# Kernel tuning notes

Measured on AMD Instinct MI355X. Metric: run time of the kernel, lower is better.

Reference implementation:

```python
import jax, jax.numpy as jnp
import numpy as np


def _tent(t):
    # linear interpolation kernel max(1-|t|, 0)
    return jnp.maximum(1.0 - jnp.abs(t), 0.0)


def _slice_coeffs(grid, guide):
    """Trilinear slice of bilateral grid at guide-dependent depth.
    grid: [B, C, D, GH, GW], guide: [B, H, W] in [0,1] -> coeffs [B, C, H, W]."""
    B, C, D, GH, GW = grid.shape
    _, H, W = guide.shape
    # continuous grid coords (HDRNet convention)
    gx = (jnp.arange(W, dtype=guide.dtype) + 0.5) * (GW / W)      # [W]
    gy = (jnp.arange(H, dtype=guide.dtype) + 0.5) * (GH / H)      # [H]
    gz = guide * D                                                # [B,H,W]
    fx = jnp.floor(gx - 0.5)
    fy = jnp.floor(gy - 0.5)
    fz = jnp.floor(gz - 0.5)

    def gather(g, z, y, x):
        # g: [C,D,GH,GW]; z,y,x: [B? broadcasted per-batch] -> [C,H,W]
        return g[:, z, y, x]

    coeffs = jnp.zeros((B, C, H, W), dtype=grid.dtype)
    ones_bhw = jnp.ones_like(gz)
    for dz in (0, 1):
        zz = fz + dz                                   # [B,H,W]
        wz = _tent(gz - 0.5 - zz)                      # [B,H,W]
        zc = jnp.clip(zz, 0, D - 1).astype(jnp.int32)
        for dy in (0, 1):
            yy = fy + dy                               # [H]
            wy = _tent(gy - 0.5 - yy)                  # [H]
            yc = jnp.clip(yy, 0, GH - 1).astype(jnp.int32)
            for dx in (0, 1):
                xx = fx + dx                           # [W]
                wx = _tent(gx - 0.5 - xx)              # [W]
                xc = jnp.clip(xx, 0, GW - 1).astype(jnp.int32)
                # broadcast indices to [B,H,W]
                Y = jnp.broadcast_to(yc[None, :, None], zc.shape)
                X = jnp.broadcast_to(xc[None, None, :], zc.shape)
                corner = jax.vmap(gather)(grid, zc, Y, X)   # [B,C,H,W]
                w = wz * wy[None, :, None] * wx[None, None, :]  # [B,H,W]
                coeffs = coeffs + corner * w[:, None, :, :]
    return coeffs


def reference(grid, guide, image):
    B, C, D, GH, GW = grid.shape
    n_out = image.shape[1]               # 3
    n_aff = C // n_out                   # n_in + 1 = 4
    coeffs = _slice_coeffs(grid, guide)  # [B, C, H, W]
    coeffs = coeffs.reshape(B, n_out, n_aff, *image.shape[2:])  # [B,3,4,H,W]
    # per-pixel affine: out_c = sum_i A[c,i] * img_i + A[c, n_in]
    out = jnp.einsum('bcihw,bihw->bchw', coeffs[:, :, : n_aff - 1], image)
    out = out + coeffs[:, :, n_aff - 1]
    return out


def setup_inputs() -> dict:
    key = jax.random.key(0)
    k1, k2, k3 = jax.random.split(key, 3)
    grid = jax.random.normal(k1, (4, 12, 8, 16, 16), dtype=jnp.float32)
    guide = jax.random.uniform(k2, (4, 1024, 1024), dtype=jnp.float32)
    image = jax.random.uniform(k3, (4, 3, 1024, 1024), dtype=jnp.float32)
    return {"grid": grid, "guide": guide, "image": image}
```

## Files before the change

### kernel.cpp

```cpp
#include <hip/hip_runtime.h>


static constexpr int C_ = 12, D_ = 8, GH_ = 16, GW_ = 16;
static constexpr int H_ = 1024, W_ = 1024;
static constexpr int HW_ = H_ * W_;
static constexpr int XS = D_ * C_ + 4;

__global__ __launch_bounds__(256) void bsa_row_kernel(
    const float* __restrict__ grid,
    const float* __restrict__ guide,
    const float* __restrict__ image,
    float* __restrict__ out)
{
    __shared__ float s[GW_ * XS];

    const int bid = blockIdx.x;
    const int y = bid & (H_ - 1);
    const int b = bid >> 10;
    const int t = threadIdx.x;

    const float gyc = (y + 0.5f) * (1.0f / 64.0f) - 0.5f;
    const float fy = floorf(gyc);
    const float ty = gyc - fy;
    const int iy = (int)fy;
    const int y0 = min(max(iy, 0), GH_ - 1);
    const int y1 = min(max(iy + 1, 0), GH_ - 1);

    const int sx = t & 15, sc = t >> 4;
    float sv0[8], sv1[8];
    const float* gb = grid + b * (C_ * D_ * GH_ * GW_);
    if (t < 192) {
        const int base = sc * (D_ * GH_ * GW_) + sx;
#pragma unroll
        for (int z = 0; z < 8; ++z) {
            sv0[z] = gb[base + z * (GH_ * GW_) + y0 * GW_];
            sv1[z] = gb[base + z * (GH_ * GW_) + y1 * GW_];
        }
    }

    const float* gdp = guide + (size_t)bid * W_;
    const float* imp = image + (size_t)b * 3 * HW_ + (size_t)y * W_;
    float gz4[4], r4[4], g4[4], b4[4];
#pragma unroll
    for (int j = 0; j < 4; ++j) {
        const int p = j * 256 + t;
        gz4[j] = gdp[p];
        r4[j]  = imp[p];
        g4[j]  = imp[HW_ + p];
        b4[j]  = imp[2 * HW_ + p];
    }

    if (t < 192) {
#pragma unroll
        for (int z = 0; z < 8; ++z)
            s[sx * XS + z * C_ + sc] = sv0[z] + ty * (sv1[z] - sv0[z]);
    }
    __syncthreads();

    float* const ob = out + (size_t)b * 3 * HW_ + (size_t)y * W_;
#pragma unroll
    for (int j = 0; j < 4; ++j) {
        const int p = j * 256 + t;

        const float gxc = (p + 0.5f) * (1.0f / 64.0f) - 0.5f;
        const float fx = floorf(gxc);
        const float tx = gxc - fx;
        const int ix = (int)fx;
        const int x0 = min(max(ix, 0), GW_ - 1);
        const int x1 = min(max(ix + 1, 0), GW_ - 1);

        const float gz = gz4[j] * (float)D_ - 0.5f;
        const float fz = floorf(gz);
        const float tz = gz - fz;
        const int iz = (int)fz;
        const int z0 = min(max(iz, 0), D_ - 1);
        const int z1 = min(max(iz + 1, 0), D_ - 1);

        const float w00 = (1.f - tx) * (1.f - tz);
        const float w01 = (1.f - tx) * tz;
        const float w10 = tx * (1.f - tz);
        const float w11 = tx * tz;

        const float* p00 = s + x0 * XS + z0 * C_;
        const float* p01 = s + x0 * XS + z1 * C_;
        const float* p10 = s + x1 * XS + z0 * C_;
        const float* p11 = s + x1 * XS + z1 * C_;

        const float rv = r4[j], gv = g4[j], bv = b4[j];

#pragma unroll
        for (int k = 0; k < 3; ++k) {
            float4 a0 = *(const float4*)(p00 + 4 * k);
            float4 a1 = *(const float4*)(p01 + 4 * k);
            float4 a2 = *(const float4*)(p10 + 4 * k);
            float4 a3 = *(const float4*)(p11 + 4 * k);
            float cx = w00 * a0.x + w01 * a1.x + w10 * a2.x + w11 * a3.x;
            float cy = w00 * a0.y + w01 * a1.y + w10 * a2.y + w11 * a3.y;
            float cz = w00 * a0.z + w01 * a1.z + w10 * a2.z + w11 * a3.z;
            float cw = w00 * a0.w + w01 * a1.w + w10 * a2.w + w11 * a3.w;
            ob[k * HW_ + p] = cx * rv + cy * gv + cz * bv + cw;
        }
    }
}

extern "C" void kernel_launch(void* const* d_in, const int* in_sizes, int n_in,
                              void* d_out, int out_size, void* d_ws, size_t ws_size,
                              hipStream_t stream) {
    const float* grid  = (const float*)d_in[0];
    const float* guide = (const float*)d_in[1];
    const float* image = (const float*)d_in[2];
    float* out = (float*)d_out;

    bsa_row_kernel<<<4 * H_, 256, 0, stream>>>(grid, guide, image, out);
}
```

Baseline: 24.44 us.

## Pack z-adjacent grid values as half2 in LDS to halve slice loads

Stores each shared-memory grid entry as a half2 holding the value at depth z and z+1, so a pixel's trilinear slice needs two 16-byte LDS reads per group of four coefficients instead of four. The z interpolation is then done from the packed pair, and the edge cases are handled by clamping z0 and zeroing tz. This cuts LDS traffic and address arithmetic in a kernel that is likely bound by memory bandwidth. In exchange it adds fp16 conversions and rounds the grid coefficients to half precision, which lowers accuracy.

```diff
diff --git a/kernel.cpp b/kernel.cpp
--- a/kernel.cpp
+++ b/kernel.cpp
@@ -1,4 +1,5 @@
 #include <hip/hip_runtime.h>
+#include <hip/hip_fp16.h>
 
 
 static constexpr int C_ = 12, D_ = 8, GH_ = 16, GW_ = 16;
@@ -6,13 +7,13 @@
 static constexpr int HW_ = H_ * W_;
 static constexpr int XS = D_ * C_ + 4;
 
-__global__ __launch_bounds__(256) void bsa_row_kernel(
+__global__ __launch_bounds__(256) void bsa_h2_kernel(
     const float* __restrict__ grid,
     const float* __restrict__ guide,
     const float* __restrict__ image,
     float* __restrict__ out)
 {
-    __shared__ float s[GW_ * XS];
+    __shared__ __half2 s[GW_ * XS];
 
     const int bid = blockIdx.x;
     const int y = bid & (H_ - 1);
@@ -51,9 +52,17 @@
     }
 
     if (t < 192) {
+        float a[8];
 #pragma unroll
         for (int z = 0; z < 8; ++z)
-            s[sx * XS + z * C_ + sc] = sv0[z] + ty * (sv1[z] - sv0[z]);
+            a[z] = sv0[z] + ty * (sv1[z] - sv0[z]);
+        const int sl = sx * XS + sc;
+#pragma unroll
+        for (int z = 0; z < 8; ++z) {
+            const int zn = (z < 7) ? z + 1 : 7;
+            s[sl + z * C_] = __halves2half2(__float2half_rn(a[z]),
+                                            __float2half_rn(a[zn]));
+        }
     }
     __syncthreads();
 
@@ -71,35 +80,37 @@
 
         const float gz = gz4[j] * (float)D_ - 0.5f;
         const float fz = floorf(gz);
-        const float tz = gz - fz;
         const int iz = (int)fz;
-        const int z0 = min(max(iz, 0), D_ - 1);
-        const int z1 = min(max(iz + 1, 0), D_ - 1);
+        const float tz = (iz < 0) ? 0.0f : (gz - fz);
+        const int z0 = max(iz, 0);
 
-        const float w00 = (1.f - tx) * (1.f - tz);
-        const float w01 = (1.f - tx) * tz;
-        const float w10 = tx * (1.f - tz);
-        const float w11 = tx * tz;
-
-        const float* p00 = s + x0 * XS + z0 * C_;
-        const float* p01 = s + x0 * XS + z1 * C_;
-        const float* p10 = s + x1 * XS + z0 * C_;
-        const float* p11 = s + x1 * XS + z1 * C_;
+        const __half2* q0 = s + x0 * XS + z0 * C_;
+        const __half2* q1 = s + x1 * XS + z0 * C_;
 
         const float rv = r4[j], gv = g4[j], bv = b4[j];
+        float res[3];
 
 #pragma unroll
         for (int k = 0; k < 3; ++k) {
-            float4 a0 = *(const float4*)(p00 + 4 * k);
-            float4 a1 = *(const float4*)(p01 + 4 * k);
-            float4 a2 = *(const float4*)(p10 + 4 * k);
-            float4 a3 = *(const float4*)(p11 + 4 * k);
-            float cx = w00 * a0.x + w01 * a1.x + w10 * a2.x + w11 * a3.x;
-            float cy = w00 * a0.y + w01 * a1.y + w10 * a2.y + w11 * a3.y;
-            float cz = w00 * a0.z + w01 * a1.z + w10 * a2.z + w11 * a3.z;
-            float cw = w00 * a0.w + w01 * a1.w + w10 * a2.w + w11 * a3.w;
-            ob[k * HW_ + p] = cx * rv + cy * gv + cz * bv + cw;
+            float4 u0 = *(const float4*)(q0 + 4 * k);
+            float4 u1 = *(const float4*)(q1 + 4 * k);
+            float c4[4];
+#pragma unroll
+            for (int e = 0; e < 4; ++e) {
+                const float ue0 = (e == 0) ? u0.x : (e == 1) ? u0.y : (e == 2) ? u0.z : u0.w;
+                const float ue1 = (e == 0) ? u1.x : (e == 1) ? u1.y : (e == 2) ? u1.z : u1.w;
+                const float2 f0 = __half22float2(__builtin_bit_cast(__half2, ue0));
+                const float2 f1 = __half22float2(__builtin_bit_cast(__half2, ue1));
+                const float v0 = fmaf(tz, f0.y - f0.x, f0.x);
+                const float v1 = fmaf(tz, f1.y - f1.x, f1.x);
+                c4[e] = fmaf(tx, v1 - v0, v0);
+            }
+            res[k] = fmaf(c4[0], rv, fmaf(c4[1], gv, fmaf(c4[2], bv, c4[3])));
         }
+
+#pragma unroll
+        for (int k = 0; k < 3; ++k)
+            ob[(size_t)k * HW_ + p] = res[k];
     }
 }
 
@@ -111,5 +122,5 @@
     const float* image = (const float*)d_in[2];
     float* out = (float*)d_out;
 
-    bsa_row_kernel<<<4 * H_, 256, 0, stream>>>(grid, guide, image, out);
+    bsa_h2_kernel<<<4 * H_, 256, 0, stream>>>(grid, guide, image, out);
 }
```

Result: slower. 27.39 us (+12.1%).
